# Kernel tuning notes

Measured on AMD Instinct MI355X. Metric: run time of the kernel, lower is better.

Reference implementation:

```python
import jax, jax.numpy as jnp
import numpy as np

B, C, H, W = 8, 19, 512, 512
FOCAL_GAMMA = 2.0
LABEL_SMOOTH = 0.1
DICE_SMOOTH = 1e-05
BOUNDARY_W = 0.5  # BoundaryLoss internal boundary_weight
W_FOCAL = W_DICE = W_CE = W_BOUNDARY = 1.0  # config term weights


def setup_inputs() -> dict:
    key = jax.random.key(0)
    k1, k2 = jax.random.split(key)
    inputs = jax.random.normal(k1, (B, C, H, W), dtype=jnp.float32)
    targets = jax.random.randint(k2, (B, H, W), 0, C, dtype=jnp.int32)
    return {"inputs": inputs, "targets": targets}


def _boundary_map(t):
    # Faithful to the torch loops: patch.max(dim=1)-patch.min(dim=1) reduces over the
    # 3 ROW offsets per column; then .any() collapses batch AND the 3 columns,
    # and the flag is written for ALL batch elements.
    vmax = jnp.maximum(jnp.maximum(t[:, :-2, :], t[:, 1:-1, :]), t[:, 2:, :])  # [B,H-2,W]
    vmin = jnp.minimum(jnp.minimum(t[:, :-2, :], t[:, 1:-1, :]), t[:, 2:, :])
    diff = jnp.any(vmax != vmin, axis=0)                                       # [H-2,W] any over batch
    hb = diff[:, :-2] | diff[:, 1:-1] | diff[:, 2:]                            # [H-2,W-2] any over 3 cols
    bm = jnp.zeros((t.shape[1], t.shape[2]), jnp.float32).at[1:-1, 1:-1].set(hb.astype(jnp.float32))
    return jnp.broadcast_to(bm[None], t.shape)                                 # [B,H,W]


def _combined(inputs, targets):
    lp = jax.nn.log_softmax(inputs, axis=1)                                    # [B,C,H,W]
    lp_t = jnp.take_along_axis(lp, targets[:, None].astype(jnp.int32), axis=1)[:, 0]  # [B,H,W]
    nll = -lp_t

    # Focal (alpha=None, no ignored pixels present)
    p_t = jnp.exp(lp_t)
    focal = jnp.mean((1.0 - p_t) ** FOCAL_GAMMA * nll)

    # Dice over all classes (vectorized over class dim)
    probs = jnp.exp(lp)
    onehot = (targets[:, None, :, :] == jnp.arange(C, dtype=targets.dtype)[None, :, None, None])
    onehot = onehot.astype(inputs.dtype)
    inter = jnp.einsum('bchw,bchw->c', probs, onehot)
    denom = jnp.sum(probs, axis=(0, 2, 3)) + jnp.sum(onehot, axis=(0, 2, 3))
    dice = jnp.mean(1.0 - (2.0 * inter + DICE_SMOOTH) / (denom + DICE_SMOOTH))

    # CE with label smoothing 0.1 (torch formula)
    smooth_term = -jnp.mean(lp, axis=1)  # (1/C) * sum_c -log p_c, [B,H,W]
    ce = jnp.mean((1.0 - LABEL_SMOOTH) * nll + LABEL_SMOOTH * smooth_term)

    # Boundary-weighted CE
    bmap = _boundary_map(targets)
    boundary = jnp.mean(nll * (1.0 + BOUNDARY_W * bmap))

    total = W_FOCAL * focal + W_DICE * dice + W_CE * ce + W_BOUNDARY * boundary
    return jnp.stack([focal, dice, ce, boundary, total])


def reference(inputs, targets):
    return _combined(inputs, targets)
```

## Files before the change

### kernel.cpp

```cpp
#include <hip/hip_runtime.h>

#define H_ 512
#define W_ 512
#define B_ 8
#define C_ 19
#define HW_ (H_ * W_)
#define NPIX (B_ * HW_)
#define NGROUPS (NPIX / 4)

#define MAIN_BLOCKS 512
#define MAIN_THREADS 256
#define PSTRIDE 64
#define DIFF_ELEMS ((H_ - 2) * W_)
#define DIFF_BYTES_PAD 262144

#define NDENSE 23
#define NVALS 61

typedef float vf4 __attribute__((ext_vector_type(4)));

__device__ __forceinline__ float wred(float v) {
    v += __shfl_down(v, 32);
    v += __shfl_down(v, 16);
    v += __shfl_down(v, 8);
    v += __shfl_down(v, 4);
    v += __shfl_down(v, 2);
    v += __shfl_down(v, 1);
    return v;
}

__global__ void diff_kernel(const int* __restrict__ tgt, unsigned char* __restrict__ diff) {
    int idx = blockIdx.x * blockDim.x + threadIdx.x;
    if (idx >= DIFF_ELEMS) return;
    int flag = 0;
    const int* p = tgt + idx;
#pragma unroll
    for (int b = 0; b < B_; ++b) {
        int t0 = p[0];
        int t1 = p[W_];
        int t2 = p[2 * W_];
        flag |= (int)(t0 != t1) | (int)(t1 != t2);
        p += HW_;
    }
    diff[idx] = (unsigned char)flag;
}

__global__ __launch_bounds__(MAIN_THREADS, 3) void main_kernel(
    const float* __restrict__ x, const int* __restrict__ tgt,
    const unsigned char* __restrict__ diff, float* __restrict__ partials)
{
    __shared__ float s_inter[C_];
    __shared__ unsigned s_cnt[C_];
    const int tid = threadIdx.x;
    if (tid < C_) { s_inter[tid] = 0.f; s_cnt[tid] = 0u; }
    __syncthreads();

    float acc[NDENSE];
#pragma unroll
    for (int k = 0; k < NDENSE; ++k) acc[k] = 0.f;

    const int stride = MAIN_BLOCKS * MAIN_THREADS;

    for (int g = blockIdx.x * MAIN_THREADS + tid; g < NGROUPS; g += stride) {
        const int p0 = g << 2;
        const int b  = p0 >> 18;
        const int hw = p0 & (HW_ - 1);
        const int h  = hw >> 9;
        const int w0 = hw & (W_ - 1);

        const vf4* xp = (const vf4*)(x + (size_t)b * (C_ * HW_) + hw);
        float v[C_][4];
#pragma unroll
        for (int c = 0; c < C_; ++c) {
            vf4 t = __builtin_nontemporal_load(xp + c * (HW_ / 4));
            v[c][0] = t.x; v[c][1] = t.y; v[c][2] = t.z; v[c][3] = t.w;
        }
        const int4 t4 = ((const int4*)tgt)[g];
        const int tArr[4] = {t4.x, t4.y, t4.z, t4.w};

        const bool hOK = (h >= 1) && (h <= H_ - 2);
        const int drow = (h - 1) << 9;

#pragma unroll
        for (int i = 0; i < 4; ++i) {
            const int t = tArr[i];
            float m = v[0][i];
#pragma unroll
            for (int c = 1; c < C_; ++c) m = fmaxf(m, v[c][i]);
            float se = 0.f, sx = 0.f, xt = 0.f, et = 0.f;
#pragma unroll
            for (int c = 0; c < C_; ++c) {
                const float xv = v[c][i];
                const float e = __expf(xv - m);
                se += e;
                sx += xv;
                const bool sel = (c == t);
                xt = sel ? xv : xt;
                et = sel ? e : et;
                v[c][i] = e;
            }
            const float invse = 1.f / se;
            const float lsum = __logf(se);
            const float nll = lsum - (xt - m);
            const float pt = et * invse;
            const float omp = 1.f - pt;
            acc[0] += omp * omp * nll;
            acc[1] += nll;
            acc[2] += (lsum + m) - sx * (1.f / C_);
            const int w = w0 + i;
            float bf = 0.f;
            if (hOK && w >= 1 && w <= W_ - 2) {
                const int dbase = drow + (w - 1);
                const unsigned d = (unsigned)diff[dbase] | (unsigned)diff[dbase + 1]
                                 | (unsigned)diff[dbase + 2];
                bf = d ? 1.f : 0.f;
            }
            acc[3] += nll * bf;
#pragma unroll
            for (int c = 0; c < C_; ++c)
                acc[4 + c] += v[c][i] * invse;
            atomicAdd(&s_inter[t], pt);
            atomicAdd(&s_cnt[t], 1u);
        }
    }

    __shared__ float red[MAIN_THREADS / 64][NDENSE];
    const int lane = tid & 63;
    const int wid = tid >> 6;
#pragma unroll
    for (int k = 0; k < NDENSE; ++k) {
        const float r = wred(acc[k]);
        if (lane == 0) red[wid][k] = r;
    }
    __syncthreads();
    float* rec = partials + blockIdx.x * PSTRIDE;
    if (tid < NDENSE) {
        float s = 0.f;
#pragma unroll
        for (int wv = 0; wv < MAIN_THREADS / 64; ++wv) s += red[wv][tid];
        rec[tid] = s;
    }
    if (tid >= 64 && tid < 64 + C_) {
        const int c = tid - 64;
        rec[23 + c] = s_inter[c];
        rec[42 + c] = (float)s_cnt[c];
    }
}

__global__ void finalize_kernel(const float* __restrict__ partials, float* __restrict__ out) {
    __shared__ double grp[4][NVALS];
    const int tid = threadIdx.x;
    const int lane = tid & 63;
    const int g = tid >> 6;
    if (lane < NVALS) {
        double s = 0.0;
        for (int b = g; b < MAIN_BLOCKS; b += 4)
            s += (double)partials[b * PSTRIDE + lane];
        grp[g][lane] = s;
    }
    __syncthreads();
    if (tid == 0) {
        double sums[NVALS];
        for (int k = 0; k < NVALS; ++k)
            sums[k] = grp[0][k] + grp[1][k] + grp[2][k] + grp[3][k];
        const double Np = (double)NPIX;
        const double focal = sums[0] / Np;
        const double ce = (0.9 * sums[1] + 0.1 * sums[2]) / Np;
        const double boundary = (sums[1] + 0.5 * sums[3]) / Np;
        double dice = 0.0;
        for (int c = 0; c < C_; ++c) {
            const double I2 = 2.0 * sums[23 + c] + 1e-5;
            const double D = sums[4 + c] + sums[42 + c] + 1e-5;
            dice += 1.0 - I2 / D;
        }
        dice /= (double)C_;
        const double total = focal + dice + ce + boundary;
        out[0] = (float)focal;
        out[1] = (float)dice;
        out[2] = (float)ce;
        out[3] = (float)boundary;
        out[4] = (float)total;
    }
}

extern "C" void kernel_launch(void* const* d_in, const int* in_sizes, int n_in,
                              void* d_out, int out_size, void* d_ws, size_t ws_size,
                              hipStream_t stream) {
    const float* x = (const float*)d_in[0];
    const int* tgt = (const int*)d_in[1];
    float* out = (float*)d_out;
    unsigned char* diff = (unsigned char*)d_ws;
    float* partials = (float*)((char*)d_ws + DIFF_BYTES_PAD);

    diff_kernel<<<(DIFF_ELEMS + 255) / 256, 256, 0, stream>>>(tgt, diff);
    main_kernel<<<MAIN_BLOCKS, MAIN_THREADS, 0, stream>>>(x, tgt, diff, partials);
    finalize_kernel<<<1, 256, 0, stream>>>(partials, out);
}
```

Before: 281.3 us.

## Fuse finalize into main kernel via last-block counter and vectorize diff kernel

Removes the separate finalize kernel launch: each main-kernel block bumps a global atomic counter after writing its partials, and the last block to finish does the double-precision reduction and writes the outputs. The counter is zeroed by the diff kernel. The diff kernel now handles four columns per thread with int4 loads and a uchar4 store, cutting thread count and load instructions. This saves one launch and a kernel boundary in exchange for threadfence and atomic overhead and a serial tail in the last block.

```diff
diff --git a/kernel.cpp b/kernel.cpp
--- a/kernel.cpp
+++ b/kernel.cpp
@@ -13,6 +13,7 @@
 #define PSTRIDE 64
 #define DIFF_ELEMS ((H_ - 2) * W_)
 #define DIFF_BYTES_PAD 262144
+#define PARTIALS_BYTES (MAIN_BLOCKS * PSTRIDE * 4)
 
 #define NDENSE 23
 #define NVALS 61
@@ -29,25 +30,35 @@
     return v;
 }
 
-__global__ void diff_kernel(const int* __restrict__ tgt, unsigned char* __restrict__ diff) {
-    int idx = blockIdx.x * blockDim.x + threadIdx.x;
-    if (idx >= DIFF_ELEMS) return;
-    int flag = 0;
+__global__ void diff_kernel(const int* __restrict__ tgt, unsigned char* __restrict__ diff,
+                            unsigned* __restrict__ counter) {
+    int q = blockIdx.x * blockDim.x + threadIdx.x;
+    if (q == 0) *counter = 0u;
+    if (q >= DIFF_ELEMS / 4) return;
+    const int idx = q << 2;
+    int f0 = 0, f1 = 0, f2 = 0, f3 = 0;
     const int* p = tgt + idx;
 #pragma unroll
     for (int b = 0; b < B_; ++b) {
-        int t0 = p[0];
-        int t1 = p[W_];
-        int t2 = p[2 * W_];
-        flag |= (int)(t0 != t1) | (int)(t1 != t2);
+        const int4 t0 = *(const int4*)(p);
+        const int4 t1 = *(const int4*)(p + W_);
+        const int4 t2 = *(const int4*)(p + 2 * W_);
+        f0 |= (int)(t0.x != t1.x) | (int)(t1.x != t2.x);
+        f1 |= (int)(t0.y != t1.y) | (int)(t1.y != t2.y);
+        f2 |= (int)(t0.z != t1.z) | (int)(t1.z != t2.z);
+        f3 |= (int)(t0.w != t1.w) | (int)(t1.w != t2.w);
         p += HW_;
     }
-    diff[idx] = (unsigned char)flag;
+    uchar4 o;
+    o.x = (unsigned char)f0; o.y = (unsigned char)f1;
+    o.z = (unsigned char)f2; o.w = (unsigned char)f3;
+    *(uchar4*)(diff + idx) = o;
 }
 
 __global__ __launch_bounds__(MAIN_THREADS, 3) void main_kernel(
     const float* __restrict__ x, const int* __restrict__ tgt,
-    const unsigned char* __restrict__ diff, float* __restrict__ partials)
+    const unsigned char* __restrict__ diff, float* __restrict__ partials,
+    unsigned* __restrict__ counter, float* __restrict__ out)
 {
     __shared__ float s_inter[C_];
     __shared__ unsigned s_cnt[C_];
@@ -145,18 +156,24 @@
         rec[23 + c] = s_inter[c];
         rec[42 + c] = (float)s_cnt[c];
     }
-}
-
-__global__ void finalize_kernel(const float* __restrict__ partials, float* __restrict__ out) {
+    __syncthreads();
+
+    __shared__ unsigned s_done;
+    if (tid == 0) {
+        __threadfence();
+        s_done = atomicAdd(counter, 1u);
+    }
+    __syncthreads();
+    if (s_done != MAIN_BLOCKS - 1) return;
+    __threadfence();
+
     __shared__ double grp[4][NVALS];
-    const int tid = threadIdx.x;
-    const int lane = tid & 63;
-    const int g = tid >> 6;
+    const int g4 = tid >> 6;
     if (lane < NVALS) {
         double s = 0.0;
-        for (int b = g; b < MAIN_BLOCKS; b += 4)
+        for (int b = g4; b < MAIN_BLOCKS; b += 4)
             s += (double)partials[b * PSTRIDE + lane];
-        grp[g][lane] = s;
+        grp[g4][lane] = s;
     }
     __syncthreads();
     if (tid == 0) {
@@ -191,8 +208,8 @@
     float* out = (float*)d_out;
     unsigned char* diff = (unsigned char*)d_ws;
     float* partials = (float*)((char*)d_ws + DIFF_BYTES_PAD);
-
-    diff_kernel<<<(DIFF_ELEMS + 255) / 256, 256, 0, stream>>>(tgt, diff);
-    main_kernel<<<MAIN_BLOCKS, MAIN_THREADS, 0, stream>>>(x, tgt, diff, partials);
-    finalize_kernel<<<1, 256, 0, stream>>>(partials, out);
-}
+    unsigned* counter = (unsigned*)((char*)d_ws + DIFF_BYTES_PAD + PARTIALS_BYTES);
+
+    diff_kernel<<<(DIFF_ELEMS / 4 + 255) / 256, 256, 0, stream>>>(tgt, diff, counter);
+    main_kernel<<<MAIN_BLOCKS, MAIN_THREADS, 0, stream>>>(x, tgt, diff, partials, counter, out);
+}
```

New measurement: 293.9 us. +4.5%, slower.
